# Kernel tuning notes

Measured on AMD Instinct MI355X. Metric: run time of the kernel, lower is better.

Reference implementation:

```python
import jax, jax.numpy as jnp
import numpy as np

B, H, S, D = 2, 16, 2048, 64

def setup_inputs() -> dict:
    key0 = jax.random.key(0)
    kq, kk, kv = jax.random.split(key0, 3)
    return {
        "query": jax.random.normal(kq, (B, H, S, D), dtype=jnp.float32),
        "key": jax.random.normal(kk, (B, H, S, D), dtype=jnp.float32),
        "value": jax.random.normal(kv, (B, H, S, D), dtype=jnp.float32),
        "inv_scale_factor": jnp.full((1,), np.sqrt(D), dtype=jnp.float32),
    }

def reference(query, key, value, inv_scale_factor):
    # qk: [B,H,S,S]
    qk = jnp.einsum("bhqd,bhkd->bhqk", query, key)
    scaled_qk = qk / inv_scale_factor
    softmax_qk = jax.nn.softmax(scaled_qk, axis=-1)
    # dropout_p = 0.0 -> identity (deterministic reference)
    out = jnp.einsum("bhqk,bhkd->bhqd", softmax_qk, value)
    return out
```

## Files before the change

### kernel.cpp

```cpp
#include <hip/hip_runtime.h>
#include <hip/hip_bf16.h>


typedef __attribute__((ext_vector_type(8))) short short8;
typedef __attribute__((ext_vector_type(16))) float floatx16;

#define SS 2048
#define DD 64
#define NITER (SS / 64)
#define LOG2E 1.44269504f

#define MFMA32(a, b, c) __builtin_amdgcn_mfma_f32_32x32x16_bf16(a, b, c, 0, 0, 0)

#define KF_SHORTS (32 * 64 * 4 * 64 * 8)
#define VF_SHORTS (32 * 64 * 4 * 64 * 8)

static __device__ inline unsigned pack2bf(float a, float b) {
    unsigned ua = __builtin_bit_cast(unsigned, a) + 0x8000u;
    unsigned ub = __builtin_bit_cast(unsigned, b) + 0x8000u;
    return __builtin_amdgcn_perm(ub, ua, 0x07060302u);
}

static __device__ inline unsigned cvtpk(float lo, float hi) {
    unsigned r;
    asm("v_cvt_pk_bf16_f32 %0, %1, %2" : "=v"(r) : "v"(lo), "v"(hi));
    return r;
}

__global__ __launch_bounds__(256)
void prepack_kernel(const float* __restrict__ K, const float* __restrict__ V,
                    short* __restrict__ Kf, short* __restrict__ Vf)
{
    int t = blockIdx.x * 256 + threadIdx.x;
    int lane = t & 63;
    int l31 = lane & 31, hi = lane >> 5;
    if (t < 524288) {
        int c = t >> 6;
        int ks = c & 3, kvb = (c >> 2) & 63, hd = c >> 8;
        const float* src = K + (size_t)hd * 131072
                             + (size_t)(kvb * 32 + l31) * 64 + ks * 16 + hi * 8;
        float4 f0 = *(const float4*)src;
        float4 f1 = *(const float4*)(src + 4);
        uint4 o;
        o.x = pack2bf(f0.x, f0.y); o.y = pack2bf(f0.z, f0.w);
        o.z = pack2bf(f1.x, f1.y); o.w = pack2bf(f1.z, f1.w);
        *(uint4*)(Kf + (size_t)t * 8) = o;
    } else {
        int u = t - 524288;
        int c = u >> 6;
        int ksl = c & 1, dt = (c >> 1) & 1, kvb = (c >> 2) & 63, hd = c >> 8;
        const float* src = V + (size_t)hd * 131072
                             + (size_t)(kvb * 32 + ksl * 16 + hi * 8) * 64
                             + dt * 32 + l31;
        float v[8];
#pragma unroll
        for (int jj = 0; jj < 8; ++jj) v[jj] = src[(size_t)jj * 64];
        uint4 o;
        o.x = pack2bf(v[0], v[1]); o.y = pack2bf(v[2], v[3]);
        o.z = pack2bf(v[4], v[5]); o.w = pack2bf(v[6], v[7]);
        *(uint4*)(Vf + (size_t)u * 8) = o;
    }
}

__global__ __launch_bounds__(256, 4)
void fattn_kernel(const float* __restrict__ Q, const short* __restrict__ Kf,
                  const short* __restrict__ Vf, const float* __restrict__ isf,
                  float* __restrict__ O)
{
    __shared__ __align__(16) char smem[17664];
    float* O_buf = (float*)smem;
    float* l_buf = (float*)(smem + 17408);
#define OSTR 68

    const int tid  = threadIdx.x;
    const int wave = tid >> 6;
    const int w_m  = wave & 1;
    const int w_n  = wave >> 1;
    const int lane = tid & 63;
    const int l31  = lane & 31;
    const int hi   = lane >> 5;

    const int b    = blockIdx.x & 1023;
    const int xcd  = b & 7;
    const int j    = b >> 3;
    const int head = xcd + 8 * (j & 3);
    const int qt   = j >> 2;

    const float scl2 = (1.0f / isf[0]) * LOG2E;

    const float* Qh = Q + (size_t)head * SS * DD;
    float*       Oh = O + (size_t)head * SS * DD;

    const short* kp = Kf + (size_t)head * 131072 + w_n * 2048 + lane * 8;
    const short* vp = Vf + (size_t)head * 131072 + w_n * 2048 + lane * 8;

    short8 kA0 = *(const short8*)(kp + 0);
    short8 kA1 = *(const short8*)(kp + 512);
    short8 kA2 = *(const short8*)(kp + 1024);
    short8 kA3 = *(const short8*)(kp + 1536);
    short8 kB0, kB1, kB2, kB3;

    short8 q_frag[4];
    {
        const float* qrow = Qh + (size_t)(qt * 64 + w_m * 32 + l31) * DD;
#pragma unroll
        for (int ks = 0; ks < 4; ++ks) {
            float4 f0 = *(const float4*)(qrow + ks * 16 + hi * 8);
            float4 f1 = *(const float4*)(qrow + ks * 16 + hi * 8 + 4);
            uint4 qp;
            qp.x = pack2bf(f0.x * scl2, f0.y * scl2);
            qp.y = pack2bf(f0.z * scl2, f0.w * scl2);
            qp.z = pack2bf(f1.x * scl2, f1.y * scl2);
            qp.w = pack2bf(f1.z * scl2, f1.w * scl2);
            q_frag[ks] = __builtin_bit_cast(short8, qp);
        }
    }

    floatx16 o_acc[2];
#pragma unroll
    for (int i = 0; i < 16; ++i) { o_acc[0][i] = 0.0f; o_acc[1][i] = 0.0f; }
    float lsum = 0.0f;

#define FBODY(K0, K1, K2, K3, V00, V01, V10, V11)                          \
    do {                                                                   \
        floatx16 s = {0.f,0.f,0.f,0.f,0.f,0.f,0.f,0.f,                     \
                      0.f,0.f,0.f,0.f,0.f,0.f,0.f,0.f};                    \
        s = MFMA32(K0, q_frag[0], s);                                      \
        s = MFMA32(K1, q_frag[1], s);                                      \
        s = MFMA32(K2, q_frag[2], s);                                      \
        s = MFMA32(K3, q_frag[3], s);                                      \
        float p[16];                                                       \
        _Pragma("unroll")                                                  \
        for (int i = 0; i < 16; ++i) p[i] = __builtin_amdgcn_exp2f(s[i]);  \
        lsum += (((p[0]+p[1])+(p[2]+p[3]))+((p[4]+p[5])+(p[6]+p[7])))      \
              + (((p[8]+p[9])+(p[10]+p[11]))+((p[12]+p[13])+(p[14]+p[15])));\
         \
        unsigned x0 = cvtpk(p[0], p[1]),   x1 = cvtpk(p[2], p[3]);         \
        unsigned y0 = cvtpk(p[4], p[5]),   y1 = cvtpk(p[6], p[7]);         \
        unsigned x2 = cvtpk(p[8], p[9]),   x3 = cvtpk(p[10], p[11]);       \
        unsigned y2 = cvtpk(p[12], p[13]), y3 = cvtpk(p[14], p[15]);       \
                              \
        unsigned f0 = __shfl_xor(hi ? x0 : y0, 32);                        \
        unsigned f1 = __shfl_xor(hi ? x1 : y1, 32);                        \
        unsigned f2 = __shfl_xor(hi ? x2 : y2, 32);                        \
        unsigned f3 = __shfl_xor(hi ? x3 : y3, 32);                        \
        uint4 B0u = { hi ? f0 : x0, hi ? f1 : x1,                          \
                      hi ? y0 : f0, hi ? y1 : f1 };    \
        uint4 B1u = { hi ? f2 : x2, hi ? f3 : x3,                          \
                      hi ? y2 : f2, hi ? y3 : f3 };   \
        short8 Bf0 = __builtin_bit_cast(short8, B0u);                      \
        short8 Bf1 = __builtin_bit_cast(short8, B1u);                      \
        o_acc[0] = MFMA32(V00, Bf0, o_acc[0]);                             \
        o_acc[1] = MFMA32(V10, Bf0, o_acc[1]);                             \
        o_acc[0] = MFMA32(V01, Bf1, o_acc[0]);                             \
        o_acc[1] = MFMA32(V11, Bf1, o_acc[1]);                             \
    } while (0)

    for (int kb = 0; kb < NITER; kb += 2) {
        short8 v00 = *(const short8*)(vp + 0);
        short8 v01 = *(const short8*)(vp + 512);
        short8 v10 = *(const short8*)(vp + 1024);
        short8 v11 = *(const short8*)(vp + 1536);
        kB0 = *(const short8*)(kp + 4096);
        kB1 = *(const short8*)(kp + 4608);
        kB2 = *(const short8*)(kp + 5120);
        kB3 = *(const short8*)(kp + 5632);
        FBODY(kA0, kA1, kA2, kA3, v00, v01, v10, v11);

        short8 w00 = *(const short8*)(vp + 4096);
        short8 w01 = *(const short8*)(vp + 4608);
        short8 w10 = *(const short8*)(vp + 5120);
        short8 w11 = *(const short8*)(vp + 5632);
        kA0 = *(const short8*)(kp + 8192);
        kA1 = *(const short8*)(kp + 8704);
        kA2 = *(const short8*)(kp + 9216);
        kA3 = *(const short8*)(kp + 9728);
        FBODY(kB0, kB1, kB2, kB3, w00, w01, w10, w11);

        kp += 8192; vp += 8192;
    }

    lsum += __shfl_xor(lsum, 32);

    const int row = w_m * 32 + l31;
    if (w_n == 1) {
#pragma unroll
        for (int dt = 0; dt < 2; ++dt)
#pragma unroll
            for (int g = 0; g < 4; ++g) {
                float4 v = { o_acc[dt][g * 4 + 0], o_acc[dt][g * 4 + 1],
                             o_acc[dt][g * 4 + 2], o_acc[dt][g * 4 + 3] };
                *(float4*)&O_buf[row * OSTR + dt * 32 + g * 8 + hi * 4] = v;
            }
        if (lane < 32) l_buf[row] = lsum;
    }
    __syncthreads();
    if (w_n == 0) {
        float lt = lsum + l_buf[row];
        float rl = 1.0f / lt;
        float* orow = Oh + (size_t)(qt * 64 + row) * DD;
#pragma unroll
        for (int dt = 0; dt < 2; ++dt)
#pragma unroll
            for (int g = 0; g < 4; ++g) {
                float4 part = *(float4*)&O_buf[row * OSTR + dt * 32 + g * 8 + hi * 4];
                float4 v;
                v.x = (o_acc[dt][g * 4 + 0] + part.x) * rl;
                v.y = (o_acc[dt][g * 4 + 1] + part.y) * rl;
                v.z = (o_acc[dt][g * 4 + 2] + part.z) * rl;
                v.w = (o_acc[dt][g * 4 + 3] + part.w) * rl;
                *(float4*)(orow + dt * 32 + g * 8 + hi * 4) = v;
            }
    }
}

extern "C" void kernel_launch(void* const* d_in, const int* in_sizes, int n_in,
                              void* d_out, int out_size, void* d_ws, size_t ws_size,
                              hipStream_t stream) {
    const float* Q   = (const float*)d_in[0];
    const float* K   = (const float*)d_in[1];
    const float* V   = (const float*)d_in[2];
    const float* isf = (const float*)d_in[3];
    float* O = (float*)d_out;

    short* Kf = (short*)d_ws;
    short* Vf = Kf + KF_SHORTS;

    prepack_kernel<<<4096, 256, 0, stream>>>(K, V, Kf, Vf);
    fattn_kernel<<<1024, 256, 0, stream>>>(Q, Kf, Vf, isf, O);
}
```

Baseline: 159.1 us.

## Batch two QK tiles per iteration and interleave softmax with PV using setprio

Result: slower. 255.8 us (+60.7%).

```diff
diff --git a/kernel.cpp b/kernel.cpp
--- a/kernel.cpp
+++ b/kernel.cpp
@@ -98,7 +98,10 @@
     short8 kA1 = *(const short8*)(kp + 512);
     short8 kA2 = *(const short8*)(kp + 1024);
     short8 kA3 = *(const short8*)(kp + 1536);
-    short8 kB0, kB1, kB2, kB3;
+    short8 kB0 = *(const short8*)(kp + 4096);
+    short8 kB1 = *(const short8*)(kp + 4608);
+    short8 kB2 = *(const short8*)(kp + 5120);
+    short8 kB3 = *(const short8*)(kp + 5632);
 
     short8 q_frag[4];
     {
@@ -121,25 +124,23 @@
     for (int i = 0; i < 16; ++i) { o_acc[0][i] = 0.0f; o_acc[1][i] = 0.0f; }
     float lsum = 0.0f;
 
-#define FBODY(K0, K1, K2, K3, V00, V01, V10, V11)                          \
+#define QK4(sv, K0, K1, K2, K3)                                            \
+    sv = MFMA32(K0, q_frag[0], sv);                                        \
+    sv = MFMA32(K1, q_frag[1], sv);                                        \
+    sv = MFMA32(K2, q_frag[2], sv);                                        \
+    sv = MFMA32(K3, q_frag[3], sv);
+
+#define SMX(sv, B0f, B1f)                                                  \
     do {                                                                   \
-        floatx16 s = {0.f,0.f,0.f,0.f,0.f,0.f,0.f,0.f,                     \
-                      0.f,0.f,0.f,0.f,0.f,0.f,0.f,0.f};                    \
-        s = MFMA32(K0, q_frag[0], s);                                      \
-        s = MFMA32(K1, q_frag[1], s);                                      \
-        s = MFMA32(K2, q_frag[2], s);                                      \
-        s = MFMA32(K3, q_frag[3], s);                                      \
         float p[16];                                                       \
         _Pragma("unroll")                                                  \
-        for (int i = 0; i < 16; ++i) p[i] = __builtin_amdgcn_exp2f(s[i]);  \
+        for (int i = 0; i < 16; ++i) p[i] = __builtin_amdgcn_exp2f((sv)[i]);\
         lsum += (((p[0]+p[1])+(p[2]+p[3]))+((p[4]+p[5])+(p[6]+p[7])))      \
               + (((p[8]+p[9])+(p[10]+p[11]))+((p[12]+p[13])+(p[14]+p[15])));\
-         \
         unsigned x0 = cvtpk(p[0], p[1]),   x1 = cvtpk(p[2], p[3]);         \
         unsigned y0 = cvtpk(p[4], p[5]),   y1 = cvtpk(p[6], p[7]);         \
         unsigned x2 = cvtpk(p[8], p[9]),   x3 = cvtpk(p[10], p[11]);       \
         unsigned y2 = cvtpk(p[12], p[13]), y3 = cvtpk(p[14], p[15]);       \
-                              \
         unsigned f0 = __shfl_xor(hi ? x0 : y0, 32);                        \
         unsigned f1 = __shfl_xor(hi ? x1 : y1, 32);                        \
         unsigned f2 = __shfl_xor(hi ? x2 : y2, 32);                        \
@@ -148,34 +149,52 @@
                       hi ? y0 : f0, hi ? y1 : f1 };    \
         uint4 B1u = { hi ? f2 : x2, hi ? f3 : x3,                          \
                       hi ? y2 : f2, hi ? y3 : f3 };   \
-        short8 Bf0 = __builtin_bit_cast(short8, B0u);                      \
-        short8 Bf1 = __builtin_bit_cast(short8, B1u);                      \
-        o_acc[0] = MFMA32(V00, Bf0, o_acc[0]);                             \
-        o_acc[1] = MFMA32(V10, Bf0, o_acc[1]);                             \
-        o_acc[0] = MFMA32(V01, Bf1, o_acc[0]);                             \
-        o_acc[1] = MFMA32(V11, Bf1, o_acc[1]);                             \
+        B0f = __builtin_bit_cast(short8, B0u);                             \
+        B1f = __builtin_bit_cast(short8, B1u);                             \
     } while (0)
+
+#define PV4(V00, V01, V10, V11, B0f, B1f)                                  \
+    o_acc[0] = MFMA32(V00, B0f, o_acc[0]);                                 \
+    o_acc[1] = MFMA32(V10, B0f, o_acc[1]);                                 \
+    o_acc[0] = MFMA32(V01, B1f, o_acc[0]);                                 \
+    o_acc[1] = MFMA32(V11, B1f, o_acc[1]);
 
     for (int kb = 0; kb < NITER; kb += 2) {
         short8 v00 = *(const short8*)(vp + 0);
         short8 v01 = *(const short8*)(vp + 512);
         short8 v10 = *(const short8*)(vp + 1024);
         short8 v11 = *(const short8*)(vp + 1536);
-        kB0 = *(const short8*)(kp + 4096);
-        kB1 = *(const short8*)(kp + 4608);
-        kB2 = *(const short8*)(kp + 5120);
-        kB3 = *(const short8*)(kp + 5632);
-        FBODY(kA0, kA1, kA2, kA3, v00, v01, v10, v11);
-
         short8 w00 = *(const short8*)(vp + 4096);
         short8 w01 = *(const short8*)(vp + 4608);
         short8 w10 = *(const short8*)(vp + 5120);
         short8 w11 = *(const short8*)(vp + 5632);
+
+        floatx16 sE = {0.f,0.f,0.f,0.f,0.f,0.f,0.f,0.f,
+                       0.f,0.f,0.f,0.f,0.f,0.f,0.f,0.f};
+        floatx16 sO = sE;
+        __builtin_amdgcn_s_setprio(1);
+        QK4(sE, kA0, kA1, kA2, kA3);
+        QK4(sO, kB0, kB1, kB2, kB3);
+        __builtin_amdgcn_s_setprio(0);
+
         kA0 = *(const short8*)(kp + 8192);
         kA1 = *(const short8*)(kp + 8704);
         kA2 = *(const short8*)(kp + 9216);
         kA3 = *(const short8*)(kp + 9728);
-        FBODY(kB0, kB1, kB2, kB3, w00, w01, w10, w11);
+        kB0 = *(const short8*)(kp + 12288);
+        kB1 = *(const short8*)(kp + 12800);
+        kB2 = *(const short8*)(kp + 13312);
+        kB3 = *(const short8*)(kp + 13824);
+
+        short8 BfE0, BfE1, BfO0, BfO1;
+        SMX(sE, BfE0, BfE1);
+        __builtin_amdgcn_s_setprio(1);
+        PV4(v00, v01, v10, v11, BfE0, BfE1);
+        __builtin_amdgcn_s_setprio(0);
+        SMX(sO, BfO0, BfO1);
+        __builtin_amdgcn_s_setprio(1);
+        PV4(w00, w01, w10, w11, BfO0, BfO1);
+        __builtin_amdgcn_s_setprio(0);
 
         kp += 8192; vp += 8192;
     }
```
